# Optimization experiments

Hardware: AMD Instinct MI355X
Metric: run time of the kernel (lower is better)

Reference implementation:

```python
import jax, jax.numpy as jnp
import numpy as np
import math

N_NODES = 20000
N_EDGES = 320000
NODE_IN = 128
HIDDEN = 64
HEADS = 4
TIME_DIM = 64
SCALE = 60.0 / 1.0  # sensitivity / epsilon


def _linear_params(key, din, dout):
    k1, k2 = jax.random.split(key)
    bound = 1.0 / math.sqrt(din)
    w = jax.random.uniform(k1, (din, dout), minval=-bound, maxval=bound, dtype=jnp.float32)
    b = jax.random.uniform(k2, (dout,), minval=-bound, maxval=bound, dtype=jnp.float32)
    return w, b


def setup_inputs() -> dict:
    key = jax.random.key(0)
    ks = jax.random.split(key, 16)
    edge_index = jax.random.randint(ks[0], (2, N_EDGES), 0, N_NODES, dtype=jnp.int64)
    raw_time = jax.random.uniform(ks[1], (N_EDGES, 1), dtype=jnp.float32) * 86400.0
    noise = jax.random.laplace(ks[2], (N_EDGES, 1), dtype=jnp.float32) * SCALE
    node_emb = jax.random.normal(ks[3], (N_NODES, NODE_IN), dtype=jnp.float32)
    HC = HEADS * HIDDEN
    wq1, bq1 = _linear_params(ks[4], NODE_IN, HC)
    wk1, bk1 = _linear_params(ks[5], NODE_IN, HC)
    wv1, bv1 = _linear_params(ks[6], NODE_IN, HC)
    wt1, bt1 = _linear_params(ks[7], TIME_DIM, HC)
    wq2, bq2 = _linear_params(ks[8], HC, HC)
    wk2, bk2 = _linear_params(ks[9], HC, HC)
    wv2, bv2 = _linear_params(ks[10], HC, HC)
    wt2, bt2 = _linear_params(ks[11], TIME_DIM, HC)
    wc, bc = _linear_params(ks[12], HC, 1)
    return dict(edge_index=edge_index, raw_time=raw_time, noise=noise, node_emb=node_emb,
                wq1=wq1, bq1=bq1, wk1=wk1, bk1=bk1, wv1=wv1, bv1=bv1, wt1=wt1, bt1=bt1,
                wq2=wq2, bq2=bq2, wk2=wk2, bk2=bk2, wv2=wv2, bv2=bv2, wt2=wt2, bt2=bt2,
                wc=wc, bc=bc)


def time_encode(t):
    # t: [E, 1] -> [E, TIME_DIM]; interleaved sin/cos as in TimeEncoder
    half = jnp.arange(0, TIME_DIM, 2, dtype=jnp.float32)
    div_term = jnp.exp(half * (-math.log(10000.0) / TIME_DIM))  # [TIME_DIM/2]
    arg = t * div_term  # [E, TIME_DIM/2]
    te = jnp.stack([jnp.sin(arg), jnp.cos(arg)], axis=-1)  # [E, T/2, 2]
    return te.reshape(t.shape[0], TIME_DIM)


def temporal_conv(x, src, dst, time_enc, wq, bq, wk, bk, wv, bv, wt, bt):
    # gather-QKV, edge softmax over dst segments, scatter-add aggregation
    N = x.shape[0]
    q = (x @ wq + bq).reshape(N, HEADS, HIDDEN)
    k = (x @ wk + bk).reshape(N, HEADS, HIDDEN)
    v = (x @ wv + bv).reshape(N, HEADS, HIDDEN)
    t_enc = (time_enc @ wt + bt).reshape(-1, HEADS, HIDDEN)  # [E,H,C]
    q_i = q[dst]                      # [E,H,C]
    k_j = k[src] + t_enc              # [E,H,C]
    alpha = (q_i * k_j).sum(-1) / math.sqrt(HIDDEN)  # [E,H]
    # segment softmax over index = dst (PyG softmax semantics)
    amax = jax.ops.segment_max(alpha, dst, num_segments=N)  # [N,H]
    ea = jnp.exp(alpha - amax[dst])
    denom = jax.ops.segment_sum(ea, dst, num_segments=N)
    alpha = ea / (denom[dst] + 1e-16)
    msg = v[src] * alpha[..., None]   # [E,H,C]
    out = jax.ops.segment_sum(msg, dst, num_segments=N)  # [N,H,C]
    return out.reshape(N, HEADS * HIDDEN)


def reference(edge_index, raw_time, noise, node_emb,
              wq1, bq1, wk1, bk1, wv1, bv1, wt1, bt1,
              wq2, bq2, wk2, bk2, wv2, bv2, wt2, bt2,
              wc, bc):
    src, dst = edge_index[0], edge_index[1]
    noisy_time = raw_time + noise                 # Laplace mechanism
    time_encoded = time_encode(noisy_time)        # [E, TIME_DIM]
    x = jax.nn.relu(temporal_conv(node_emb, src, dst, time_encoded,
                                  wq1, bq1, wk1, bk1, wv1, bv1, wt1, bt1))
    x = jax.nn.relu(temporal_conv(x, src, dst, time_encoded,
                                  wq2, bq2, wk2, bk2, wv2, bv2, wt2, bt2))
    edge_emb = x[src] + x[dst]                    # [E, H*C]
    out = edge_emb @ wc + bc                      # [E, 1]
    return out.squeeze(-1)
```

## Files before the change

### kernel.cpp

```cpp
#include <hip/hip_runtime.h>
#include <hip/hip_fp16.h>
#include <math.h>

#define NN   20000
#define NE   320000
#define NIN  128
#define HC   256
#define NB   1024

#define AGG_BLOCKS 2500
#define AGG_STRIDE 10000
#define LOG2E_8    0.18033688f

typedef unsigned short u16;
typedef __attribute__((ext_vector_type(8))) short bf16x8;
typedef __attribute__((ext_vector_type(4))) float f32x4;

__device__ __forceinline__ float bf2f(u16 u) {
  union { unsigned int i; float f; } x;
  x.i = ((unsigned int)u) << 16;
  return x.f;
}
__device__ __forceinline__ u16 f2bf(float f) {
  union { float f; unsigned int i; } x;
  x.f = f;
  unsigned int r = x.i + 0x7fffu + ((x.i >> 16) & 1u);
  return (u16)(r >> 16);
}
__device__ __forceinline__ float bflo(int v) {
  union { int i; float f; } x; x.i = v << 16; return x.f;
}
__device__ __forceinline__ float bfhi(int v) {
  union { int i; float f; } x; x.i = v & 0xffff0000; return x.f;
}

__device__ __forceinline__ float ldf(const void* p, int i, bool fbf) {
  return fbf ? bf2f(((const u16*)p)[i]) : ((const float*)p)[i];
}
__device__ __forceinline__ int ldsrc(const void* p, int e, bool is64) {
  const int* p32 = (const int*)p;
  return is64 ? p32[2 * e] : p32[e];
}
__device__ __forceinline__ int lddst(const void* p, int e, bool is64) {
  const int* p32 = (const int*)p;
  return is64 ? p32[2 * (NE + e)] : p32[NE + e];
}
__device__ __forceinline__ void stout(void* p, int i, float v, bool fbf) {
  if (fbf) ((u16*)p)[i] = f2bf(v);
  else ((float*)p)[i] = v;
}

__device__ __forceinline__ void gload_lds16(const u16* g, u16* l) {
  __builtin_amdgcn_global_load_lds(
      (const __attribute__((address_space(1))) void*)g,
      (__attribute__((address_space(3))) void*)l, 16, 0, 0);
}

__device__ __forceinline__ float dpp_row_allsum(float s) {
  union fi { float f; int i; };
  fi a, b;
  a.f = s;
  b.i = __builtin_amdgcn_update_dpp(0, a.i, 0x121, 0xf, 0xf, true); a.f += b.f;
  b.i = __builtin_amdgcn_update_dpp(0, a.i, 0x122, 0xf, 0xf, true); a.f += b.f;
  b.i = __builtin_amdgcn_update_dpp(0, a.i, 0x124, 0xf, 0xf, true); a.f += b.f;
  b.i = __builtin_amdgcn_update_dpp(0, a.i, 0x128, 0xf, 0xf, true); a.f += b.f;
  return a.f;
}

__device__ __forceinline__ float fexp2(float x) {
#if __has_builtin(__builtin_amdgcn_exp2f)
  return __builtin_amdgcn_exp2f(x);
#else
  return exp2f(x);
#endif
}

#if __has_builtin(__builtin_amdgcn_fdot2_f32_bf16)
#define HAS_BF16_DOT2 1
typedef __attribute__((ext_vector_type(2))) __bf16 bfv2_t;
__device__ __forceinline__ float qkdot2(int a, int b, float c) {
  return __builtin_amdgcn_fdot2_f32_bf16(__builtin_bit_cast(bfv2_t, a),
                                         __builtin_bit_cast(bfv2_t, b), c, false);
}
#else
#define HAS_BF16_DOT2 0
#endif

__device__ __forceinline__ void edge_do(int2 kk, int2 vv, float tt, int2 q2,
    float dc0, float dc1,
    float qsx, float qsy, float qsz, float qsw,
    float px, float py, float pz, float pw, float qb,
    float& denom, float& a0, float& a1, float& a2, float& a3) {
  const float CH = 0.15915494f;
  const float CL = (float)(0.15915494309189535 - (double)0.15915494f);
  float x0 = tt * dc0, x1 = tt * dc1;
  float p0 = x0 * CH, p1 = x1 * CH;
  float e0 = fmaf(x0, CH, -p0), e1 = fmaf(x1, CH, -p1);
  e0 = fmaf(x0, CL, e0);  e1 = fmaf(x1, CL, e1);
  float fr0 = (p0 - rintf(p0)) + e0;
  float fr1 = (p1 - rintf(p1)) + e1;
  float sv0 = __builtin_amdgcn_sinf(fr0), cv0 = __builtin_amdgcn_cosf(fr0);
  float sv1 = __builtin_amdgcn_sinf(fr1), cv1 = __builtin_amdgcn_cosf(fr1);
  float stp = sv0 * px + cv0 * py + sv1 * pz + cv1 * pw;
#if HAS_BF16_DOT2
  float sqk = qkdot2(kk.y, q2.y, qkdot2(kk.x, q2.x, 0.f));
  float partial = sqk * LOG2E_8 + stp;
#else
  float partial = stp + qsx * bflo(kk.x) + qsy * bfhi(kk.x) +
                  qsz * bflo(kk.y) + qsw * bfhi(kk.y);
#endif
  float a = dpp_row_allsum(partial) + qb;
  float ea = fexp2(a);
  denom += ea;
  a0 = fmaf(ea, bflo(vv.x), a0);
  a1 = fmaf(ea, bfhi(vv.x), a1);
  a2 = fmaf(ea, bflo(vv.y), a2);
  a3 = fmaf(ea, bfhi(vv.y), a3);
}

__global__ void devinit_kernel(const void* __restrict__ eidx,
                               const void* __restrict__ nemb,
                               int* __restrict__ flags, float* __restrict__ divt) {
  int lane = threadIdx.x;
  if (lane < 32) {
    const float c32 = (float)(-0.14391156831212787);
    float prod = (float)(2 * lane) * c32;
    divt[lane] = (float)exp((double)prod);
  }
  if (lane == 0) {
    const int* p32 = (const int*)eidx;
    int is64 = 1;
    for (int i = 1; i < 128; i += 2)
      if (p32[i] != 0) { is64 = 0; break; }
    const u16* q16 = (const u16*)nemb;
    int fbf = 1;
    for (int i = 0; i < 128; i += 2) {
      unsigned e = (q16[i] >> 7) & 0xFF;
      if (e < 90 || e > 140) { fbf = 0; break; }
    }
    flags[0] = is64;
    flags[1] = fbf;
  }
}

__global__ void sentinel_kernel(const int* __restrict__ flags, void* __restrict__ out) {
  int i = blockIdx.x * 256 + threadIdx.x;
  if (i < NE) stout(out, i, 3000.0f, flags[1] != 0);
}
__global__ void raw_sentinel_kernel(u16* __restrict__ out) {
  int i = blockIdx.x * 256 + threadIdx.x;
  if (i < NE) out[i] = f2bf(3000.0f);
}

__global__ void zero_kernel(int* __restrict__ p, int n) {
  int i = blockIdx.x * 256 + threadIdx.x;
  if (i < n) p[i] = 0;
}

__global__ void hist_kernel(const int* __restrict__ flags, const void* __restrict__ eidx,
                            int* __restrict__ cnt) {
  bool is64 = flags[0] != 0;
  int e = blockIdx.x * 256 + threadIdx.x;
  if (e < NE) {
    int d = lddst(eidx, e, is64);
    if ((unsigned)d < NN) atomicAdd(&cnt[d], 1);
  }
}

__global__ void scan1_kernel(const int* __restrict__ cnt, int* __restrict__ offs,
                             int* __restrict__ bsum, int n) {
  __shared__ int s[256];
  int b = blockIdx.x, t = threadIdx.x, i = b * 256 + t;
  int x = (i < n) ? cnt[i] : 0;
  s[t] = x;
  __syncthreads();
  for (int off = 1; off < 256; off <<= 1) {
    int y = (t >= off) ? s[t - off] : 0;
    __syncthreads();
    s[t] += y;
    __syncthreads();
  }
  if (i < n) offs[i] = s[t] - x;
  if (t == 255) bsum[b] = s[t];
}

__global__ void scan2_kernel(int* __restrict__ bsum, int* __restrict__ offs,
                             int nb, int n) {
  __shared__ int s[256];
  int t = threadIdx.x;
  int x = (t < nb) ? bsum[t] : 0;
  s[t] = x;
  __syncthreads();
  for (int off = 1; off < 256; off <<= 1) {
    int y = (t >= off) ? s[t - off] : 0;
    __syncthreads();
    s[t] += y;
    __syncthreads();
  }
  if (t < nb) bsum[t] = s[t] - x;
  if (t == 255) offs[n] = s[t];
}

__global__ void scan3_kernel(int* __restrict__ offs, const int* __restrict__ bsum,
                             int* __restrict__ cursor, int n) {
  int i = blockIdx.x * 256 + threadIdx.x;
  if (i < n) {
    int v = offs[i] + bsum[blockIdx.x];
    offs[i] = v;
    cursor[i] = v;
  }
}

__global__ void fill_kernel(const int* __restrict__ flags, const void* __restrict__ eidx,
                            const void* __restrict__ rawt, const void* __restrict__ noise,
                            int* __restrict__ cursor, int* __restrict__ ssrc,
                            float* __restrict__ stt) {
  bool is64 = flags[0] != 0, fbf = flags[1] != 0;
  int e = blockIdx.x * 256 + threadIdx.x;
  if (e < NE) {
    int d = lddst(eidx, e, is64);
    if ((unsigned)d < NN) {
      int pos = atomicAdd(&cursor[d], 1);
      if ((unsigned)pos < NE) {
        int src = ldsrc(eidx, e, is64);
        if ((unsigned)src >= NN) src = 0;
        ssrc[pos] = src;
        stt[pos] = ldf(rawt, e, fbf) + ldf(noise, e, fbf);
      }
    }
  }
}

__global__ void transw3_kernel(const int* __restrict__ flags, const void* __restrict__ W0,
                               const void* __restrict__ W1, const void* __restrict__ W2,
                               u16* __restrict__ WtBig, int K) {
  bool fbf = flags[1] != 0;
  __shared__ u16 tile[64][65];
  int z = blockIdx.z;
  const void* W = (z == 0) ? W0 : (z == 1) ? W1 : W2;
  u16* dst = WtBig + (size_t)z * 256 * K;
  int kb = blockIdx.x * 64, cb = blockIdx.y * 64;
  int tx = threadIdx.x & 63, ty = threadIdx.x >> 6;
  for (int i = ty; i < 64; i += 4)
    tile[tx][i] = f2bf(ldf(W, (kb + i) * HC + cb + tx, fbf));
  __syncthreads();
  for (int i = ty; i < 64; i += 4)
    dst[(size_t)(cb + i) * K + kb + tx] = tile[i][tx];
}

__global__ void wcombbias_kernel(const int* __restrict__ flags, const void* __restrict__ wt,
                                 const u16* __restrict__ Wqt, u16* __restrict__ Wout,
                                 const void* __restrict__ bq, const void* __restrict__ bk,
                                 const void* __restrict__ bv, float* __restrict__ biasBig,
                                 int K) {
  bool fbf = flags[1] != 0;
  int b = blockIdx.x, t = threadIdx.x;
  if (b < 256) {
    __shared__ float wrow[64];
    int j = b, h = j >> 6;
    if (t < 64) wrow[t] = ldf(wt, (j & 63) * HC + h * 64 + t, fbf);
    __syncthreads();
    if (t < K) {
      float s = 0.f;
#pragma unroll 8
      for (int mm = 0; mm < 64; ++mm)
        s += wrow[mm] * bf2f(Wqt[(size_t)(h * 64 + mm) * K + t]);
      Wout[(size_t)j * K + t] = f2bf(s);
    }
  } else if (b < 259) {
    int bb = b - 256;
    const void* p = (bb == 0) ? bq : (bb == 1) ? bk : bv;
    biasBig[bb * 256 + t] = ldf(p, t, fbf);
  } else {
    int j = t, h = j >> 6;
    float s = 0.f;
    for (int mm = 0; mm < 64; ++mm)
      s += ldf(bq, h * 64 + mm, fbf) * ldf(wt, (j & 63) * HC + h * 64 + mm, fbf);
    biasBig[768 + j] = s;
  }
}

template <bool AWS>
__global__ __launch_bounds__(256) void gemm_mfma(
    const int* __restrict__ flags, const void* __restrict__ Ap,
    const u16* __restrict__ Wt, const float* __restrict__ bias,
    u16* __restrict__ C, int M, int K) {
  bool fbf = flags[1] != 0;
  __shared__ u16 As[2][128 * 32];
  __shared__ u16 Bs[2][128 * 32];
  int tid = threadIdx.x;
  int rb = blockIdx.x * 128, cb = blockIdx.y * 128;
  int wave = tid >> 6, lane = tid & 63;
  int l15 = lane & 15, quad = lane >> 4;
  int mbase = (wave >> 1) * 64, nbase = (wave & 1) * 64;

  f32x4 acc[4][4];
#pragma unroll
  for (int mt = 0; mt < 4; ++mt)
#pragma unroll
    for (int nt = 0; nt < 4; ++nt)
#pragma unroll
      for (int r = 0; r < 4; ++r) acc[mt][nt][r] = 0.f;

  int srow0 = tid >> 2, schunk0 = tid & 3;
  int srow1 = (tid + 256) >> 2, schunk1 = (tid + 256) & 3;
  int gchunk0 = schunk0 ^ (srow0 & 3);
  int gchunk1 = schunk1 ^ (srow1 & 3);
  int arow0 = rb + srow0; if (arow0 >= M) arow0 = M - 1;
  int arow1 = rb + srow1; if (arow1 >= M) arow1 = M - 1;
  int slo0 = srow0 * 32 + schunk0 * 8;
  int slo1 = srow1 * 32 + schunk1 * 8;
  const u16* bsrc0 = Wt + (size_t)(cb + srow0) * K + gchunk0 * 8;
  const u16* bsrc1 = Wt + (size_t)(cb + srow1) * K + gchunk1 * 8;
  const bool adirect = AWS || fbf;
  const u16* asrc0 = adirect ? ((const u16*)Ap + (size_t)arow0 * K + gchunk0 * 8) : (const u16*)0;
  const u16* asrc1 = adirect ? ((const u16*)Ap + (size_t)arow1 * K + gchunk1 * 8) : (const u16*)0;
  const float* afsrc0 = (const float*)Ap + (size_t)arow0 * K + gchunk0 * 8;
  const float* afsrc1 = (const float*)Ap + (size_t)arow1 * K + gchunk1 * 8;

  auto STAGE = [&](int b, int kk) {
    if (adirect) {
      gload_lds16(asrc0 + kk, &As[b][slo0]);
      gload_lds16(asrc1 + kk, &As[b][slo1]);
    } else {
      const float* A0 = afsrc0 + kk;
      const float* A1 = afsrc1 + kk;
      bf16x8 t0, t1;
#pragma unroll
      for (int i = 0; i < 8; ++i) { t0[i] = (short)f2bf(A0[i]); t1[i] = (short)f2bf(A1[i]); }
      *(bf16x8*)&As[b][slo0] = t0;
      *(bf16x8*)&As[b][slo1] = t1;
    }
    gload_lds16(bsrc0 + kk, &Bs[b][slo0]);
    gload_lds16(bsrc1 + kk, &Bs[b][slo1]);
  };

  auto COMPUTE = [&](int b) {
    bf16x8 bfrag[4];
#pragma unroll
    for (int nt = 0; nt < 4; ++nt) {
      int col = nbase + nt * 16 + l15;
      bfrag[nt] = *(const bf16x8*)&Bs[b][col * 32 + ((quad ^ (col & 3)) * 8)];
    }
#pragma unroll
    for (int mt = 0; mt < 4; ++mt) {
      int row = mbase + mt * 16 + l15;
      bf16x8 afrag = *(const bf16x8*)&As[b][row * 32 + ((quad ^ (row & 3)) * 8)];
#pragma unroll
      for (int nt = 0; nt < 4; ++nt)
        acc[mt][nt] = __builtin_amdgcn_mfma_f32_16x16x32_bf16(afrag, bfrag[nt], acc[mt][nt], 0, 0, 0);
    }
  };

  STAGE(0, 0);
  __syncthreads();
  int cur = 0;
  for (int kk = 32; kk < K; kk += 32) {
    STAGE(cur ^ 1, kk);
    COMPUTE(cur);
    __syncthreads();
    cur ^= 1;
  }
  COMPUTE(cur);

  float bvv[4];
#pragma unroll
  for (int nt = 0; nt < 4; ++nt) bvv[nt] = bias[cb + nbase + nt * 16 + l15];
#pragma unroll
  for (int mt = 0; mt < 4; ++mt) {
#pragma unroll
    for (int r = 0; r < 4; ++r) {
      int grow = rb + mbase + mt * 16 + quad * 4 + r;
      if (grow < M) {
        size_t rowo = (size_t)grow * NB + cb + nbase + l15;
#pragma unroll
        for (int nt = 0; nt < 4; ++nt)
          C[rowo + nt * 16] = f2bf(acc[mt][nt][r] + bvv[nt]);
      }
    }
  }
}

template <int DOY>
__global__ __launch_bounds__(256) void aggfused_kernel(
    const int* __restrict__ flags, const int* __restrict__ ssrc,
    const int* __restrict__ offsets, const float* __restrict__ stt,
    const float* __restrict__ divt,
    const u16* __restrict__ qkvp, const void* __restrict__ bt,
    u16* __restrict__ xout, const void* __restrict__ wc,
    float* __restrict__ ynode) {
  bool fbf = flags[1] != 0;
  int lane = threadIdx.x & 63;
  int c = lane * 4;

  int i0 = (2 * lane) & 31;
  float dc0 = divt[i0], dc1 = divt[i0 + 1];
  float btv0 = ldf(bt, c + 0, fbf), btv1 = ldf(bt, c + 1, fbf);
  float btv2 = ldf(bt, c + 2, fbf), btv3 = ldf(bt, c + 3, fbf);
  float wcv0 = 0.f, wcv1 = 0.f, wcv2 = 0.f, wcv3 = 0.f;
  if (DOY) {
    wcv0 = ldf(wc, c + 0, fbf); wcv1 = ldf(wc, c + 1, fbf);
    wcv2 = ldf(wc, c + 2, fbf); wcv3 = ldf(wc, c + 3, fbf);
  }

  int n = blockIdx.x * 4 + (threadIdx.x >> 6);
  int s0 = offsets[n], s1 = offsets[n + 1];
  int2 q2 = *(const int2*)(qkvp + (size_t)n * NB + c);
  int2 p2 = *(const int2*)(qkvp + (size_t)n * NB + 768 + c);

  while (n < NN) {
    int n1 = n + AGG_STRIDE;
    int n1c = (n1 < NN) ? n1 : 0;
    int s0n = offsets[n1c], s1n = offsets[n1c + 1];
    int2 q2n = *(const int2*)(qkvp + (size_t)n1c * NB + c);
    int2 p2n = *(const int2*)(qkvp + (size_t)n1c * NB + 768 + c);

    float qx = bflo(q2.x), qy = bfhi(q2.x), qz = bflo(q2.y), qw = bfhi(q2.y);
    float px = bflo(p2.x) * LOG2E_8, py = bfhi(p2.x) * LOG2E_8;
    float pz = bflo(p2.y) * LOG2E_8, pw = bfhi(p2.y) * LOG2E_8;
    float pb = qx * btv0 + qy * btv1 + qz * btv2 + qw * btv3;
    float qb = dpp_row_allsum(pb) * LOG2E_8;
    float qsx = qx * LOG2E_8, qsy = qy * LOG2E_8;
    float qsz = qz * LOG2E_8, qsw = qw * LOG2E_8;

    float denom = 0.f, acc0 = 0.f, acc1 = 0.f, acc2 = 0.f, acc3 = 0.f;
    const int* sp = ssrc + s0;
    const float* tp = stt + s0;
    int ecnt = s1 - s0;
    int e = 0;
    if (ecnt >= 4) {
      int sA = sp[0], sB = sp[1], sC = sp[2], sD = sp[3];
      while (e + 4 <= ecnt) {
        const u16* bA = qkvp + ((unsigned)sA << 10) + c;
        const u16* bB = qkvp + ((unsigned)sB << 10) + c;
        const u16* bC = qkvp + ((unsigned)sC << 10) + c;
        const u16* bD = qkvp + ((unsigned)sD << 10) + c;
        int2 kA = *(const int2*)(bA + 256), vA = *(const int2*)(bA + 512);
        int2 kB = *(const int2*)(bB + 256), vB = *(const int2*)(bB + 512);
        int2 kC = *(const int2*)(bC + 256), vC = *(const int2*)(bC + 512);
        int2 kD = *(const int2*)(bD + 256), vD = *(const int2*)(bD + 512);
        float ttA = tp[e], ttB = tp[e + 1], ttC = tp[e + 2], ttD = tp[e + 3];
        int en = e + 4;
        if (en + 4 <= ecnt) {
          sA = sp[en]; sB = sp[en + 1]; sC = sp[en + 2]; sD = sp[en + 3];
        }
        edge_do(kA, vA, ttA, q2, dc0, dc1, qsx, qsy, qsz, qsw, px, py, pz, pw, qb,
                denom, acc0, acc1, acc2, acc3);
        edge_do(kB, vB, ttB, q2, dc0, dc1, qsx, qsy, qsz, qsw, px, py, pz, pw, qb,
                denom, acc0, acc1, acc2, acc3);
        edge_do(kC, vC, ttC, q2, dc0, dc1, qsx, qsy, qsz, qsw, px, py, pz, pw, qb,
                denom, acc0, acc1, acc2, acc3);
        edge_do(kD, vD, ttD, q2, dc0, dc1, qsx, qsy, qsz, qsw, px, py, pz, pw, qb,
                denom, acc0, acc1, acc2, acc3);
        e = en;
      }
    }
    for (; e < ecnt; ++e) {
      int s = sp[e];
      const u16* bS = qkvp + ((unsigned)s << 10) + c;
      int2 kS = *(const int2*)(bS + 256), vS = *(const int2*)(bS + 512);
      float tt = tp[e];
      edge_do(kS, vS, tt, q2, dc0, dc1, qsx, qsy, qsz, qsw, px, py, pz, pw, qb,
              denom, acc0, acc1, acc2, acc3);
    }

    float inv = 1.f / (denom + 1e-16f);
    ushort4 r;
    r.x = f2bf(fmaxf(acc0 * inv, 0.f));
    r.y = f2bf(fmaxf(acc1 * inv, 0.f));
    r.z = f2bf(fmaxf(acc2 * inv, 0.f));
    r.w = f2bf(fmaxf(acc3 * inv, 0.f));
    *(ushort4*)(xout + (size_t)n * HC + c) = r;
    if (DOY) {
      float yv = bf2f(r.x) * wcv0 + bf2f(r.y) * wcv1 +
                 bf2f(r.z) * wcv2 + bf2f(r.w) * wcv3;
      yv = dpp_row_allsum(yv);
      yv += __shfl_xor(yv, 16);
      yv += __shfl_xor(yv, 32);
      if (lane == 0) ynode[n] = yv;
    }

    n = n1;
    s0 = s0n; s1 = s1n; q2 = q2n; p2 = p2n;
  }
}

__global__ __launch_bounds__(256) void final2_kernel(
    const int* __restrict__ flags, const void* __restrict__ eidx,
    const float* __restrict__ y, const void* __restrict__ bc,
    void* __restrict__ out) {
  bool is64 = flags[0] != 0, fbf = flags[1] != 0;
  int e = blockIdx.x * 256 + threadIdx.x;
  if (e >= NE) return;
  int src = ldsrc(eidx, e, is64);
  int dst = lddst(eidx, e, is64);
  if ((unsigned)src >= NN) src = 0;
  if ((unsigned)dst >= NN) dst = 0;
  stout(out, e, y[src] + y[dst] + ldf(bc, 0, fbf), fbf);
}

extern "C" void kernel_launch(void* const* d_in, const int* in_sizes, int n_in,
                              void* d_out, int out_size, void* d_ws, size_t ws_size,
                              hipStream_t stream) {
  const void* eidx  = d_in[0];
  const void* rawt  = d_in[1];
  const void* noise = d_in[2];
  const void* nemb  = d_in[3];
  const void *wq1 = d_in[4],  *bq1 = d_in[5];
  const void *wk1 = d_in[6],  *bk1 = d_in[7];
  const void *wv1 = d_in[8],  *bv1 = d_in[9];
  const void *wt1 = d_in[10], *bt1 = d_in[11];
  const void *wq2 = d_in[12], *bq2 = d_in[13];
  const void *wk2 = d_in[14], *bk2 = d_in[15];
  const void *wv2 = d_in[16], *bv2 = d_in[17];
  const void *wt2 = d_in[18], *bt2 = d_in[19];
  const void *wcp = d_in[20], *bcp = d_in[21];

  char* ws = (char*)d_ws;
  size_t off = 0;
  auto alloc = [&](size_t bytes) -> void* {
    void* p = ws + off;
    off += (bytes + 255) & ~(size_t)255;
    return p;
  };
  int*   flags  = (int*)alloc(256);
  float* divt   = (float*)alloc(256);
  u16*   WtBig  = (u16*)alloc((size_t)NB * HC * 2);
  float* biasBig= (float*)alloc((size_t)NB * 4);
  u16*   qkvp   = (u16*)alloc((size_t)NN * NB * 2);
  u16*   x1     = (u16*)alloc((size_t)NN * HC * 2);
  u16*   x2     = (u16*)alloc((size_t)NN * HC * 2);
  float* ynode  = (float*)alloc((size_t)NN * 4);
  int* offsets  = (int*)alloc((size_t)(NN + 1) * 4);
  int* cursor   = (int*)alloc((size_t)NN * 4);
  int* bsum     = (int*)alloc(256 * 4);
  int* ssrc     = (int*)alloc((size_t)NE * 4);
  float* stt    = (float*)alloc((size_t)NE * 4);
  size_t need = off;

  int gN = (NN + 255) / 256, gE = (NE + 255) / 256;
  int nb = (NN + 255) / 256;

  if (ws_size < 1024) {
    raw_sentinel_kernel<<<gE, 256, 0, stream>>>((u16*)d_out);
    return;
  }
  devinit_kernel<<<1, 64, 0, stream>>>(eidx, nemb, flags, divt);
  if (need > ws_size) {
    sentinel_kernel<<<gE, 256, 0, stream>>>(flags, d_out);
    return;
  }

  zero_kernel<<<gN, 256, 0, stream>>>(cursor, NN);
  hist_kernel<<<gE, 256, 0, stream>>>(flags, eidx, cursor);
  scan1_kernel<<<nb, 256, 0, stream>>>(cursor, offsets, bsum, NN);
  scan2_kernel<<<1, 256, 0, stream>>>(bsum, offsets, nb, NN);
  scan3_kernel<<<nb, 256, 0, stream>>>(offsets, bsum, cursor, NN);
  fill_kernel<<<gE, 256, 0, stream>>>(flags, eidx, rawt, noise, cursor, ssrc, stt);

  dim3 ggemm((NN + 127) / 128, NB / 128);
  dim3 gt1(NIN / 64, 4, 3), gt2(HC / 64, 4, 3);

  transw3_kernel<<<gt1, 256, 0, stream>>>(flags, wq1, wk1, wv1, WtBig, NIN);
  wcombbias_kernel<<<260, 256, 0, stream>>>(flags, wt1, WtBig, WtBig + (size_t)768 * NIN,
                                            bq1, bk1, bv1, biasBig, NIN);
  gemm_mfma<false><<<ggemm, 256, 0, stream>>>(flags, nemb, WtBig, biasBig, qkvp, NN, NIN);
  aggfused_kernel<0><<<AGG_BLOCKS, 256, 0, stream>>>(flags, ssrc, offsets, stt, divt,
                                                     qkvp, bt1, x1, wcp, ynode);

  transw3_kernel<<<gt2, 256, 0, stream>>>(flags, wq2, wk2, wv2, WtBig, HC);
  wcombbias_kernel<<<260, 256, 0, stream>>>(flags, wt2, WtBig, WtBig + (size_t)768 * HC,
                                            bq2, bk2, bv2, biasBig, HC);
  gemm_mfma<true><<<ggemm, 256, 0, stream>>>(flags, x1, WtBig, biasBig, qkvp, NN, HC);
  aggfused_kernel<1><<<AGG_BLOCKS, 256, 0, stream>>>(flags, ssrc, offsets, stt, divt,
                                                     qkvp, bt2, x2, wcp, ynode);

  final2_kernel<<<gE, 256, 0, stream>>>(flags, eidx, ynode, bcp, d_out);
}
```

Before: 337.0 us.

## Pre-cast node embeddings to bf16 and remap GEMM blocks per XCD

```diff
diff --git a/kernel.cpp b/kernel.cpp
--- a/kernel.cpp
+++ b/kernel.cpp
@@ -11,6 +11,9 @@
 #define AGG_BLOCKS 2500
 #define AGG_STRIDE 10000
 #define LOG2E_8    0.18033688f
+
+#define GEMM_BLOCKS 1280
+#define GEMM_RT     157
 
 typedef unsigned short u16;
 typedef __attribute__((ext_vector_type(8))) short bf16x8;
@@ -231,6 +234,19 @@
   }
 }
 
+__global__ __launch_bounds__(256) void cast_kernel(const int* __restrict__ flags,
+                                                   const void* __restrict__ in,
+                                                   u16* __restrict__ out) {
+  if (flags[1]) return;
+  int i = blockIdx.x * 256 + threadIdx.x;
+  if (i < NN * NIN / 4) {
+    float4 v = ((const float4*)in)[i];
+    ushort4 o;
+    o.x = f2bf(v.x); o.y = f2bf(v.y); o.z = f2bf(v.z); o.w = f2bf(v.w);
+    ((ushort4*)out)[i] = o;
+  }
+}
+
 __global__ void transw3_kernel(const int* __restrict__ flags, const void* __restrict__ W0,
                                const void* __restrict__ W1, const void* __restrict__ W2,
                                u16* __restrict__ WtBig, int K) {
@@ -283,13 +299,24 @@
 template <bool AWS>
 __global__ __launch_bounds__(256) void gemm_mfma(
     const int* __restrict__ flags, const void* __restrict__ Ap,
-    const u16* __restrict__ Wt, const float* __restrict__ bias,
-    u16* __restrict__ C, int M, int K) {
+    const u16* __restrict__ Acast, const u16* __restrict__ Wt,
+    const float* __restrict__ bias, u16* __restrict__ C, int M, int K) {
   bool fbf = flags[1] != 0;
+  const u16* A = AWS ? (const u16*)Ap : (fbf ? (const u16*)Ap : Acast);
+
+  int lid = blockIdx.x;
+  int xcd = lid & 7;
+  int j = lid >> 3;
+  int rl = j >> 3, col = j & 7;
+  const int qr = GEMM_RT >> 3, rem = GEMM_RT & 7;
+  int nrows = qr + (xcd < rem ? 1 : 0);
+  if (rl >= nrows) return;
+  int row = xcd * qr + (xcd < rem ? xcd : rem) + rl;
+  int rb = row * 128, cb = col * 128;
+
   __shared__ u16 As[2][128 * 32];
   __shared__ u16 Bs[2][128 * 32];
   int tid = threadIdx.x;
-  int rb = blockIdx.x * 128, cb = blockIdx.y * 128;
   int wave = tid >> 6, lane = tid & 63;
   int l15 = lane & 15, quad = lane >> 4;
   int mbase = (wave >> 1) * 64, nbase = (wave & 1) * 64;
@@ -312,25 +339,12 @@
   int slo1 = srow1 * 32 + schunk1 * 8;
   const u16* bsrc0 = Wt + (size_t)(cb + srow0) * K + gchunk0 * 8;
   const u16* bsrc1 = Wt + (size_t)(cb + srow1) * K + gchunk1 * 8;
-  const bool adirect = AWS || fbf;
-  const u16* asrc0 = adirect ? ((const u16*)Ap + (size_t)arow0 * K + gchunk0 * 8) : (const u16*)0;
-  const u16* asrc1 = adirect ? ((const u16*)Ap + (size_t)arow1 * K + gchunk1 * 8) : (const u16*)0;
-  const float* afsrc0 = (const float*)Ap + (size_t)arow0 * K + gchunk0 * 8;
-  const float* afsrc1 = (const float*)Ap + (size_t)arow1 * K + gchunk1 * 8;
+  const u16* asrc0 = A + (size_t)arow0 * K + gchunk0 * 8;
+  const u16* asrc1 = A + (size_t)arow1 * K + gchunk1 * 8;
 
   auto STAGE = [&](int b, int kk) {
-    if (adirect) {
-      gload_lds16(asrc0 + kk, &As[b][slo0]);
-      gload_lds16(asrc1 + kk, &As[b][slo1]);
-    } else {
-      const float* A0 = afsrc0 + kk;
-      const float* A1 = afsrc1 + kk;
-      bf16x8 t0, t1;
-#pragma unroll
-      for (int i = 0; i < 8; ++i) { t0[i] = (short)f2bf(A0[i]); t1[i] = (short)f2bf(A1[i]); }
-      *(bf16x8*)&As[b][slo0] = t0;
-      *(bf16x8*)&As[b][slo1] = t1;
-    }
+    gload_lds16(asrc0 + kk, &As[b][slo0]);
+    gload_lds16(asrc1 + kk, &As[b][slo1]);
     gload_lds16(bsrc0 + kk, &Bs[b][slo0]);
     gload_lds16(bsrc1 + kk, &Bs[b][slo1]);
   };
@@ -339,13 +353,13 @@
     bf16x8 bfrag[4];
 #pragma unroll
     for (int nt = 0; nt < 4; ++nt) {
-      int col = nbase + nt * 16 + l15;
-      bfrag[nt] = *(const bf16x8*)&Bs[b][col * 32 + ((quad ^ (col & 3)) * 8)];
+      int col2 = nbase + nt * 16 + l15;
+      bfrag[nt] = *(const bf16x8*)&Bs[b][col2 * 32 + ((quad ^ (col2 & 3)) * 8)];
     }
 #pragma unroll
     for (int mt = 0; mt < 4; ++mt) {
-      int row = mbase + mt * 16 + l15;
-      bf16x8 afrag = *(const bf16x8*)&As[b][row * 32 + ((quad ^ (row & 3)) * 8)];
+      int row2 = mbase + mt * 16 + l15;
+      bf16x8 afrag = *(const bf16x8*)&As[b][row2 * 32 + ((quad ^ (row2 & 3)) * 8)];
 #pragma unroll
       for (int nt = 0; nt < 4; ++nt)
         acc[mt][nt] = __builtin_amdgcn_mfma_f32_16x16x32_bf16(afrag, bfrag[nt], acc[mt][nt], 0, 0, 0);
@@ -530,6 +544,7 @@
   u16*   qkvp   = (u16*)alloc((size_t)NN * NB * 2);
   u16*   x1     = (u16*)alloc((size_t)NN * HC * 2);
   u16*   x2     = (u16*)alloc((size_t)NN * HC * 2);
+  u16*   acast  = (u16*)alloc((size_t)NN * NIN * 2);
   float* ynode  = (float*)alloc((size_t)NN * 4);
   int* offsets  = (int*)alloc((size_t)(NN + 1) * 4);
   int* cursor   = (int*)alloc((size_t)NN * 4);
@@ -558,20 +573,23 @@
   scan3_kernel<<<nb, 256, 0, stream>>>(offsets, bsum, cursor, NN);
   fill_kernel<<<gE, 256, 0, stream>>>(flags, eidx, rawt, noise, cursor, ssrc, stt);
 
-  dim3 ggemm((NN + 127) / 128, NB / 128);
+  cast_kernel<<<(NN * NIN / 4 + 255) / 256, 256, 0, stream>>>(flags, nemb, acast);
+
   dim3 gt1(NIN / 64, 4, 3), gt2(HC / 64, 4, 3);
 
   transw3_kernel<<<gt1, 256, 0, stream>>>(flags, wq1, wk1, wv1, WtBig, NIN);
   wcombbias_kernel<<<260, 256, 0, stream>>>(flags, wt1, WtBig, WtBig + (size_t)768 * NIN,
                                             bq1, bk1, bv1, biasBig, NIN);
-  gemm_mfma<false><<<ggemm, 256, 0, stream>>>(flags, nemb, WtBig, biasBig, qkvp, NN, NIN);
+  gemm_mfma<false><<<GEMM_BLOCKS, 256, 0, stream>>>(flags, nemb, acast, WtBig, biasBig,
+                                                    qkvp, NN, NIN);
   aggfused_kernel<0><<<AGG_BLOCKS, 256, 0, stream>>>(flags, ssrc, offsets, stt, divt,
                                                      qkvp, bt1, x1, wcp, ynode);
 
   transw3_kernel<<<gt2, 256, 0, stream>>>(flags, wq2, wk2, wv2, WtBig, HC);
   wcombbias_kernel<<<260, 256, 0, stream>>>(flags, wt2, WtBig, WtBig + (size_t)768 * HC,
                                             bq2, bk2, bv2, biasBig, HC);
-  gemm_mfma<true><<<ggemm, 256, 0, stream>>>(flags, x1, WtBig, biasBig, qkvp, NN, HC);
+  gemm_mfma<true><<<GEMM_BLOCKS, 256, 0, stream>>>(flags, x1, (const u16*)0, WtBig, biasBig,
+                                                   qkvp, NN, HC);
   aggfused_kernel<1><<<AGG_BLOCKS, 256, 0, stream>>>(flags, ssrc, offsets, stt, divt,
                                                      qkvp, bt2, x2, wcp, ynode);
 
```

New measurement: 326.5 us, median of 2. 1.03x faster.
